# Kernel tuning notes

Hardware: AMD Instinct MI355X
Metric: run time of the kernel (lower is better)

The kernel has to match this reference:

```python
import jax, jax.numpy as jnp
import numpy as np

R = 0.9        # ball-query radius
K = 32         # max neighbors per ball
STRIDE = 4     # spatial stride -> M = N // STRIDE reference points
EPS = 1e-5     # BatchNorm eps


def fps(xyz, m):
    """Furthest point sampling (pointnet2 semantics: start at index 0).
    xyz: (N,3) -> (m,) int32 indices."""
    N = xyz.shape[0]

    def step(carry, _):
        dist, last = carry
        d = jnp.sum((xyz - xyz[last]) ** 2, axis=-1)
        dist = jnp.minimum(dist, d)
        nxt = jnp.argmax(dist).astype(jnp.int32)
        return (dist, nxt), nxt

    init = (jnp.full((N,), 1e10, dtype=xyz.dtype), jnp.int32(0))
    _, rest = jax.lax.scan(step, init, None, length=m - 1)
    return jnp.concatenate([jnp.zeros((1,), jnp.int32), rest])


def sample_group(xyz):
    """FPS + ball query + grouping for one frame. xyz: (N,3).
    Returns ref (M,3), disp4 (M,K,4)."""
    N = xyz.shape[0]
    m = N // STRIDE
    fi = fps(xyz, m)
    ref = xyz[fi]                                              # (M,3)
    d2 = jnp.sum((ref[:, None, :] - xyz[None, :, :]) ** 2, -1)  # (M,N)
    # pointnet2 ball_query: first K in-radius indices (original order),
    # positions without a neighbor padded with the first found index.
    cand = jnp.where(d2 < R * R, jnp.arange(N, dtype=jnp.int32)[None, :], N)
    idx = jnp.sort(cand, axis=1)[:, :K]                        # (M,K)
    idx = jnp.where(idx == N, idx[:, :1], idx)
    nb = xyz[idx]                                              # (M,K,3)
    disp = nb - ref[:, None, :]
    disp4 = jnp.concatenate([disp, jnp.zeros_like(disp[..., :1])], axis=-1)
    return ref, disp4


def batch_norm(h, gamma, beta):
    # torch BN (training-mode) per frame: stats over (B, M, K) per t.
    # h: (B,T,M,K,C)
    mean = jnp.mean(h, axis=(0, 2, 3), keepdims=True)
    var = jnp.mean((h - mean) ** 2, axis=(0, 2, 3), keepdims=True)
    return gamma * (h - mean) * jax.lax.rsqrt(var + EPS) + beta


def setup_inputs() -> dict:
    key = jax.random.key(0)
    ks = jax.random.split(key, 7)
    B, T, N = 2, 8, 4096
    C1, C2 = 64, 128
    return {
        "xyzs": jax.random.normal(ks[0], (B, T, N, 3), dtype=jnp.float32),
        "W1": jax.random.normal(ks[1], (C1, 4), dtype=jnp.float32) * 0.1,
        "g1": jnp.ones((C1,), jnp.float32),
        "b1": jnp.zeros((C1,), jnp.float32),
        "W2": jax.random.normal(ks[2], (C2, C1), dtype=jnp.float32) * 0.1,
        "g2": jnp.ones((C2,), jnp.float32),
        "b2": jnp.zeros((C2,), jnp.float32),
    }


def reference(xyzs, W1, g1, b1, W2, g2, b2):
    # xyzs: (B,T,N,3)
    ref, disp4 = jax.vmap(jax.vmap(sample_group))(xyzs)  # (B,T,M,3), (B,T,M,K,4)
    h = jnp.einsum('btmkc,oc->btmko', disp4, W1)         # conv_d 1x1
    h = jax.nn.relu(batch_norm(h, g1, b1))
    h = jnp.einsum('btmkc,oc->btmko', h, W2)             # mlp 1x1
    h = jax.nn.relu(batch_norm(h, g2, b2))
    feat = jnp.max(h, axis=3)                            # max over K -> (B,T,M,C)
    new_features = jnp.transpose(feat, (0, 1, 3, 2))     # (B,T,C,M) like torch
    return ref, new_features
```

## Files before the change

kernel.cpp:

```cpp
#include <hip/hip_runtime.h>
#include <hip/hip_bf16.h>


#define N_PTS   4096
#define M_PTS   1024
#define KNB     32

typedef _Float16 half8 __attribute__((ext_vector_type(8)));
typedef float    f32x4 __attribute__((ext_vector_type(4)));

__device__ inline float2 pk_sub(float2 a, float2 b) {
  float2 d;
  asm("v_pk_add_f32 %0, %1, %2 neg_lo:[0,1] neg_hi:[0,1]" : "=v"(d) : "v"(a), "v"(b));
  return d;
}
__device__ inline float2 pk_mul(float2 a, float2 b) {
  float2 d;
  asm("v_pk_mul_f32 %0, %1, %2" : "=v"(d) : "v"(a), "v"(b));
  return d;
}
__device__ inline float2 pk_add(float2 a, float2 b) {
  float2 d;
  asm("v_pk_add_f32 %0, %1, %2" : "=v"(d) : "v"(a), "v"(b));
  return d;
}

#define DPPMAXF(ctrl)                                                          \
  {                                                                            \
    unsigned _o = (unsigned)__builtin_amdgcn_update_dpp(                       \
        0, (int)__float_as_uint(m), (ctrl), 0xF, 0xF, true);                   \
    m = fmaxf(m, __uint_as_float(_o));                                         \
  }

__device__ inline float4 fold1_chan(const float* __restrict__ acc9, int t, int c,
                                    const float* __restrict__ W1,
                                    const float* __restrict__ g1,
                                    const float* __restrict__ b1) {
  const float inv_n = 1.0f / 65536.0f;
  const float* a = acc9 + t * 9;
  float mx = a[0] * inv_n, my = a[1] * inv_n, mz = a[2] * inv_n;
  float Sxx = a[3] * inv_n, Syy = a[4] * inv_n, Szz = a[5] * inv_n;
  float Sxy = a[6] * inv_n, Sxz = a[7] * inv_n, Syz = a[8] * inv_n;
  float w0 = W1[c * 4], w1 = W1[c * 4 + 1], w2 = W1[c * 4 + 2];
  float mean = w0 * mx + w1 * my + w2 * mz;
  float E2 = w0 * w0 * Sxx + w1 * w1 * Syy + w2 * w2 * Szz
           + 2.f * (w0 * w1 * Sxy + w0 * w2 * Sxz + w1 * w2 * Syz);
  float var = E2 - mean * mean;
  float al = g1[c] / sqrtf(var + 1e-5f);
  float4 o; o.x = w0 * al; o.y = w1 * al; o.z = w2 * al; o.w = b1[c] - mean * al;
  return o;
}

__global__ __launch_bounds__(512) void fps_kernel(const float* __restrict__ xyzs,
                                                  float* __restrict__ out) {
#pragma clang fp contract(off)
  const int bt  = blockIdx.x & 15;
  const int tid = threadIdx.x;
  __shared__ float sx[N_PTS], syy[N_PTS], szz[N_PTS];
  __shared__ unsigned long long sslot[2];
  __shared__ int sidx[M_PTS];

  const float* f = xyzs + (size_t)bt * (N_PTS * 3);
  for (int i = tid; i < N_PTS; i += 512) {
    sx[i]  = f[3 * i + 0];
    syy[i] = f[3 * i + 1];
    szz[i] = f[3 * i + 2];
  }
  if (tid == 0) { sidx[0] = 0; sslot[0] = 0ull; sslot[1] = 0ull; }
  __syncthreads();

  const int base = tid << 3;
  float2 px2[4], py2[4], pz2[4], dd2[4];
#pragma unroll
  for (int j = 0; j < 4; ++j) {
    int i0 = base + 2 * j;
    px2[j] = {sx[i0], sx[i0 + 1]};
    py2[j] = {syy[i0], syy[i0 + 1]};
    pz2[j] = {szz[i0], szz[i0 + 1]};
    dd2[j] = {1e10f, 1e10f};
  }
  float wx = sx[0], wy = syy[0], wz = szz[0];

  for (int it = 1; it < M_PTS; ++it) {
    float2 wxx = {wx, wx}, wyy = {wy, wy}, wzz = {wz, wz};
#pragma unroll
    for (int j = 0; j < 4; ++j) {
      float2 dx = pk_sub(px2[j], wxx);
      float2 dy = pk_sub(py2[j], wyy);
      float2 dz = pk_sub(pz2[j], wzz);
      float2 m1 = pk_mul(dx, dx);
      float2 m2 = pk_mul(dy, dy);
      float2 s  = pk_add(m1, m2);
      float2 m3 = pk_mul(dz, dz);
      float2 dt = pk_add(s, m3);
      dd2[j].x = fminf(dd2[j].x, dt.x);
      dd2[j].y = fminf(dd2[j].y, dt.y);
    }
    float v4[4]; int s4[4];
#pragma unroll
    for (int a = 0; a < 4; ++a) {
      bool t = dd2[a].y > dd2[a].x;
      v4[a] = t ? dd2[a].y : dd2[a].x;
      s4[a] = 2 * a + (t ? 1 : 0);
    }
    float v2[2]; int s2v[2];
#pragma unroll
    for (int a = 0; a < 2; ++a) {
      bool t = v4[2 * a + 1] > v4[2 * a];
      v2[a] = t ? v4[2 * a + 1] : v4[2 * a];
      s2v[a] = t ? s4[2 * a + 1] : s4[2 * a];
    }
    bool t1 = v2[1] > v2[0];
    float bv = t1 ? v2[1] : v2[0];
    int   bj = t1 ? s2v[1] : s2v[0];

    float m = bv;
    DPPMAXF(0x111);
    DPPMAXF(0x112);
    DPPMAXF(0x114);
    DPPMAXF(0x118);
    DPPMAXF(0x142);
    DPPMAXF(0x143);
    float vmax = __uint_as_float(
        (unsigned)__builtin_amdgcn_readlane((int)__float_as_uint(m), 63));

    const int p = it & 1;
    if (bv == vmax) {
      unsigned long long key = ((unsigned long long)(unsigned)it << 44)
          | ((unsigned long long)__float_as_uint(bv) << 12)
          | (unsigned long long)(4095u - (unsigned)((tid << 3) + bj));
      atomicMax(&sslot[p], key);
    }
    __syncthreads();
    unsigned long long kk = sslot[p];
    int bi = 4095 - (int)(kk & 0xFFFull);
    wx = sx[bi]; wy = syy[bi]; wz = szz[bi];
    if (tid == 0) sidx[it] = bi;
  }
  __syncthreads();
  float* orow = out + (size_t)bt * (M_PTS * 3);
  for (int i = tid; i < M_PTS; i += 512) {
    int ix = sidx[i];
    orow[3 * i + 0] = sx[ix];
    orow[3 * i + 1] = syy[ix];
    orow[3 * i + 2] = szz[ix];
  }
}

__global__ __launch_bounds__(256) void ball_stats(const float* __restrict__ xyzs,
                                                  const float* __restrict__ refpts,
                                                  float* __restrict__ disp4,
                                                  float* __restrict__ acc9) {
#pragma clang fp contract(off)
  const int tid  = threadIdx.x;
  const int lane = tid & 63, w = tid >> 6;
  const int gw   = (blockIdx.x << 2) + w;
  const int bt   = gw >> 10;
  const float* f = xyzs + (size_t)bt * (N_PTS * 3);
  const float* r = refpts + (size_t)gw * 3;
  const float rx = r[0], ry = r[1], rz = r[2];
  float* dout = disp4 + (size_t)gw * (KNB * 4);
  __shared__ float sred[4][9];

  float st[9];
#pragma unroll
  for (int q = 0; q < 9; ++q) st[q] = 0.f;

  int filled = 0;
  float p0x = 0.f, p0y = 0.f, p0z = 0.f;
  bool got0 = false;

  for (int base = 0; base < N_PTS; base += 64) {
    if (filled >= KNB) break;
    int j = base + lane;
    float x = f[3 * j], y = f[3 * j + 1], z = f[3 * j + 2];
    float dx = rx - x, dy = ry - y, dz = rz - z;
    float d2 = (dx * dx + dy * dy) + dz * dz;
    bool pred = d2 < 0.81f;
    unsigned long long mk = __ballot(pred);
    if (!got0 && mk) {
      int src = __builtin_ctzll(mk);
      p0x = __shfl(-dx, src); p0y = __shfl(-dy, src); p0z = __shfl(-dz, src);
      got0 = true;
    }
    int slot = filled + __popcll(mk & ((1ull << lane) - 1));
    if (pred && slot < KNB) {
      float vx = -dx, vy = -dy, vz = -dz;
      float4 v; v.x = vx; v.y = vy; v.z = vz; v.w = 0.f;
      *(float4*)(dout + slot * 4) = v;
      st[0] += vx;      st[1] += vy;      st[2] += vz;
      st[3] += vx * vx; st[4] += vy * vy; st[5] += vz * vz;
      st[6] += vx * vy; st[7] += vx * vz; st[8] += vy * vz;
    }
    filled += __popcll(mk);
  }
  if (filled < KNB) {
    for (int s = filled + lane; s < KNB; s += 64) {
      float4 v; v.x = p0x; v.y = p0y; v.z = p0z; v.w = 0.f;
      *(float4*)(dout + s * 4) = v;
    }
    if (lane == 0) {
      float cf = (float)(KNB - filled);
      st[0] += cf * p0x;       st[1] += cf * p0y;       st[2] += cf * p0z;
      st[3] += cf * p0x * p0x; st[4] += cf * p0y * p0y; st[5] += cf * p0z * p0z;
      st[6] += cf * p0x * p0y; st[7] += cf * p0x * p0z; st[8] += cf * p0y * p0z;
    }
  }
#pragma unroll
  for (int q = 0; q < 9; ++q) {
#pragma unroll
    for (int off = 1; off < 64; off <<= 1) st[q] += __shfl_xor(st[q], off);
  }
  if (lane == 0) {
#pragma unroll
    for (int q = 0; q < 9; ++q) sred[w][q] = st[q];
  }
  __syncthreads();
  if (tid < 9) {
    float v = sred[0][tid] + sred[1][tid] + sred[2][tid] + sred[3][tid];
    atomicAdd(&acc9[(bt & 7) * 9 + tid], v);
  }
}

__global__ __launch_bounds__(256) void gram_mfma(
    const float* __restrict__ disp4, const float* __restrict__ acc9,
    const float* __restrict__ W1, const float* __restrict__ g1,
    const float* __restrict__ b1,
    float* __restrict__ sumy, float* __restrict__ G) {
  const int t = blockIdx.x >> 5, chunk = blockIdx.x & 31;
  const int tid = threadIdx.x;
  const int lane = tid & 63, w = tid >> 6;
  __shared__ float4    sdisp[32];
  __shared__ _Float16  yt[2048];
  __shared__ float     red[256];

  const int c = lane;
  float4 wc = fold1_chan(acc9, t, c, W1, g1, b1);
  const int wswz = w ^ (c & 3) ^ ((c >> 2) & 3) ^ ((c >> 4) & 3);
  _Float16* wp = (_Float16*)((char*)yt + c * 64 + wswz * 16);

  f32x4 g0 = {0.f,0.f,0.f,0.f}, g1a = {0.f,0.f,0.f,0.f};
  f32x4 g2a = {0.f,0.f,0.f,0.f}, g3 = {0.f,0.f,0.f,0.f};
  float ysum = 0.f;

  const int frc = lane & 15, kg = lane >> 4;
  const int fsw = kg ^ (lane & 3) ^ ((lane >> 2) & 3);

  for (int b = 0; b < 64; ++b) {
    int sb = (chunk << 11) + (b << 5);
    if (tid < 32) {
      int smp = sb + tid;
      size_t flat = ((size_t)(smp >> 15) << 18) + ((size_t)t << 15) + (smp & 32767);
      sdisp[tid] = ((const float4*)disp4)[flat];
    }
    __syncthreads();
    half8 hv;
#pragma unroll
    for (int u = 0; u < 8; ++u) {
      float4 d = sdisp[w * 8 + u];
      float y = wc.x * d.x + wc.y * d.y + wc.z * d.z + wc.w;
      y = y > 0.f ? y : 0.f;
      ysum += y;
      hv[u] = (_Float16)y;
    }
    *(half8*)wp = hv;
    __syncthreads();
    half8 fA = *(const half8*)((const char*)yt + (16 * w + frc) * 64 + ((fsw ^ w) * 16));
    half8 f0 = *(const half8*)((const char*)yt + (frc) * 64       + ((fsw ^ 0) * 16));
    half8 f1 = *(const half8*)((const char*)yt + (16 + frc) * 64  + ((fsw ^ 1) * 16));
    half8 f2 = *(const half8*)((const char*)yt + (32 + frc) * 64  + ((fsw ^ 2) * 16));
    half8 f3 = *(const half8*)((const char*)yt + (48 + frc) * 64  + ((fsw ^ 3) * 16));
    g0  = __builtin_amdgcn_mfma_f32_16x16x32_f16(fA, f0, g0, 0, 0, 0);
    g1a = __builtin_amdgcn_mfma_f32_16x16x32_f16(fA, f1, g1a, 0, 0, 0);
    g2a = __builtin_amdgcn_mfma_f32_16x16x32_f16(fA, f2, g2a, 0, 0, 0);
    g3  = __builtin_amdgcn_mfma_f32_16x16x32_f16(fA, f3, g3, 0, 0, 0);
    __syncthreads();
  }
  red[tid] = ysum;
  __syncthreads();
  if (tid < 64) {
    float v = red[tid] + red[tid + 64] + red[tid + 128] + red[tid + 192];
    atomicAdd(&sumy[t * 64 + tid], v);
  }
  float* Gp = G + t * 4096;
  const int rbase = 16 * w + (lane >> 4) * 4, cb = lane & 15;
#pragma unroll
  for (int r2 = 0; r2 < 4; ++r2) {
    atomicAdd(&Gp[(rbase + r2) * 64 + cb],      g0[r2]);
    atomicAdd(&Gp[(rbase + r2) * 64 + 16 + cb], g1a[r2]);
    atomicAdd(&Gp[(rbase + r2) * 64 + 32 + cb], g2a[r2]);
    atomicAdd(&Gp[(rbase + r2) * 64 + 48 + cb], g3[r2]);
  }
}

__global__ __launch_bounds__(256) void fold2_kernel(const float* __restrict__ G,
    const float* __restrict__ sumy, const float* __restrict__ W2,
    const float* __restrict__ g2, const float* __restrict__ b2,
    _Float16* __restrict__ w2ph, float* __restrict__ beta2) {
  const int gidx = blockIdx.x * 256 + threadIdx.x;
  const int t = gidx >> 7, c2 = gidx & 127;
  const float inv_n = 1.f / 65536.f;
  const float* w = W2 + c2 * 64;
  float wreg[64];
#pragma unroll
  for (int q = 0; q < 16; ++q) {
    float4 v = ((const float4*)w)[q];
    wreg[4 * q] = v.x; wreg[4 * q + 1] = v.y; wreg[4 * q + 2] = v.z; wreg[4 * q + 3] = v.w;
  }
  float mean2 = 0.f;
#pragma unroll
  for (int j = 0; j < 64; ++j) mean2 += wreg[j] * (sumy[t * 64 + j] * inv_n);
  const float* Gp = G + t * 4096;
  float E2 = 0.f;
  for (int i = 0; i < 64; ++i) {
    const float* gr = Gp + i * 64;
    float gw = 0.f;
#pragma unroll
    for (int j = 0; j < 64; j += 4) {
      float4 gv = *(const float4*)&gr[j];
      gw += gv.x * wreg[j] + gv.y * wreg[j + 1] + gv.z * wreg[j + 2] + gv.w * wreg[j + 3];
    }
    E2 += wreg[i] * gw;
  }
  E2 *= inv_n;
  float var = E2 - mean2 * mean2;
  float al = g2[c2] / sqrtf(var + 1e-5f);
  float be = b2[c2] - mean2 * al;
  beta2[t * 128 + c2] = be;
  _Float16* wo = w2ph + (size_t)(t * 128 + c2) * 64;
#pragma unroll
  for (int j = 0; j < 64; ++j) wo[j] = (_Float16)(al * wreg[j]);
}

__global__ __launch_bounds__(256) void final_mfma(
    const float* __restrict__ disp4, const float* __restrict__ acc9,
    const float* __restrict__ W1, const float* __restrict__ g1,
    const float* __restrict__ b1,
    const _Float16* __restrict__ w2ph, const float* __restrict__ beta2,
    float* __restrict__ outfeat) {
  const int bid = blockIdx.x;
  const int bt = bid >> 6, mg = bid & 63;
  const int t = bt & 7;
  const int tid = threadIdx.x;
  const int lane = tid & 63, w = tid >> 6;

  __shared__ float4    sdisp[512];
  __shared__ _Float16  sy[512 * 64];

  {
    const float4* src = (const float4*)disp4 + (((size_t)(bt << 10) + (mg << 4)) << 5);
    sdisp[tid] = src[tid];
    sdisp[tid + 256] = src[tid + 256];
  }
  const int c0 = (tid & 31) * 2;
  float4 w1a = fold1_chan(acc9, t, c0, W1, g1, b1);
  float4 w1b = fold1_chan(acc9, t, c0 + 1, W1, g1, b1);
  __syncthreads();

  {
    const int r0 = (tid >> 5) * 64;
    const int hg = c0 >> 3;
    const int cin = (c0 & 7) * 2;
#pragma unroll 4
    for (int rr = 0; rr < 64; ++rr) {
      int row = r0 + rr;
      float4 d = sdisp[row];
      float ya = fmaxf(w1a.x * d.x + w1a.y * d.y + w1a.z * d.z + w1a.w, 0.f);
      float yb = fmaxf(w1b.x * d.x + w1b.y * d.y + w1b.z * d.z + w1b.w, 0.f);
      _Float16* p = (_Float16*)((char*)sy + row * 128 + ((hg ^ (row & 7)) * 16) + cin);
      p[0] = (_Float16)ya;
      p[1] = (_Float16)yb;
    }
  }
  __syncthreads();

  const int col = lane & 15, kg = lane >> 4;
  for (int ct = 0; ct < 8; ++ct) {
    const _Float16* wb = w2ph + ((size_t)(t * 128 + ct * 16 + col)) * 64 + kg * 8;
    half8 bf0 = *(const half8*)wb;
    half8 bf1 = *(const half8*)(wb + 32);
    float b2v = beta2[t * 128 + ct * 16 + col];
#pragma unroll
    for (int mi = 0; mi < 4; ++mi) {
      float mx = -1e30f;
#pragma unroll
      for (int h = 0; h < 2; ++h) {
        int row = (8 * w + 2 * mi + h) * 16 + col;
        int rm = row & 7;
        const char* rb = (const char*)sy + row * 128;
        half8 a0 = *(const half8*)(rb + ((kg ^ rm) * 16));
        half8 a1 = *(const half8*)(rb + (((4 + kg) ^ rm) * 16));
        f32x4 acc = {0.f, 0.f, 0.f, 0.f};
        acc = __builtin_amdgcn_mfma_f32_16x16x32_f16(a0, bf0, acc, 0, 0, 0);
        acc = __builtin_amdgcn_mfma_f32_16x16x32_f16(a1, bf1, acc, 0, 0, 0);
        float z = fmaxf(fmaxf(acc[0], acc[1]), fmaxf(acc[2], acc[3]));
        mx = fmaxf(mx, z);
      }
      mx = fmaxf(mx, __shfl_xor(mx, 16));
      mx = fmaxf(mx, __shfl_xor(mx, 32));
      if (lane < 16) {
        float v = fmaxf(mx + b2v, 0.f);
        int m = (mg << 4) + 4 * w + mi;
        outfeat[((size_t)(bt * 128 + ct * 16 + lane)) * 1024 + m] = v;
      }
    }
  }
}

extern "C" void kernel_launch(void* const* d_in, const int* in_sizes, int n_in,
                              void* d_out, int out_size, void* d_ws, size_t ws_size,
                              hipStream_t stream) {
  const float* xyzs = (const float*)d_in[0];
  const float* W1   = (const float*)d_in[1];
  const float* g1   = (const float*)d_in[2];
  const float* b1   = (const float*)d_in[3];
  const float* W2   = (const float*)d_in[4];
  const float* g2   = (const float*)d_in[5];
  const float* b2   = (const float*)d_in[6];
  float* out = (float*)d_out;
  float* ws  = (float*)d_ws;

  float*     disp4 = ws;
  float*     acc   = ws + 2097152;
  float*     sumy  = ws + 2097224;
  float*     G     = ws + 2097736;
  _Float16*  w2ph  = (_Float16*)(ws + 2130504);
  float*     beta2 = ws + 2163272;

  hipMemsetAsync(acc, 0, (72 + 512 + 32768) * sizeof(float), stream);
  fps_kernel  <<<256,  512, 0, stream>>>(xyzs, out);
  ball_stats  <<<4096, 256, 0, stream>>>(xyzs, out, disp4, acc);
  gram_mfma   <<<256,  256, 0, stream>>>(disp4, acc, W1, g1, b1, sumy, G);
  fold2_kernel<<<4,    256, 0, stream>>>(G, sumy, W2, g2, b2, w2ph, beta2);
  final_mfma  <<<1024, 256, 0, stream>>>(disp4, acc, W1, g1, b1, w2ph, beta2, out + 49152);
}
```

Measured before the change: 996.0 us.

## Broadcast FPS winner coords via LDS; enlarge gram_mfma tile to 256 samples

In FPS, the first lane of each wave that holds that wave's maximum writes its candidate coordinates to a small LDS array. After the barrier, every thread picks the winning wave's coordinates from that array instead of doing a dependent lookup into the point arrays with the winning index. In gram_mfma, each iteration now loads 256 samples instead of 32, with a larger LDS tile and a new swizzle. This runs 8 MFMA k-steps per barrier pair and cuts the loop from 64 to 8 rounds, reducing synchronisation overhead at the cost of more LDS use, which may lower occupancy.

Result: slower. 2.472 ms (+148.2%).

```diff
diff --git a/kernel.cpp b/kernel.cpp
--- a/kernel.cpp
+++ b/kernel.cpp
@@ -58,6 +58,7 @@
   const int tid = threadIdx.x;
   __shared__ float sx[N_PTS], syy[N_PTS], szz[N_PTS];
   __shared__ unsigned long long sslot[2];
+  __shared__ float4 scand[2][8];
   __shared__ int sidx[M_PTS];
 
   const float* f = xyzs + (size_t)bt * (N_PTS * 3);
@@ -124,18 +125,42 @@
     float vmax = __uint_as_float(
         (unsigned)__builtin_amdgcn_readlane((int)__float_as_uint(m), 63));
 
+    unsigned long long mk = __ballot(bv == vmax);
     const int p = it & 1;
-    if (bv == vmax) {
+    if ((tid & 63) == (int)__builtin_ctzll(mk)) {
+      float2 ax = (bj & 4) ? ((bj & 2) ? px2[3] : px2[2])
+                           : ((bj & 2) ? px2[1] : px2[0]);
+      float2 ay = (bj & 4) ? ((bj & 2) ? py2[3] : py2[2])
+                           : ((bj & 2) ? py2[1] : py2[0]);
+      float2 az = (bj & 4) ? ((bj & 2) ? pz2[3] : pz2[2])
+                           : ((bj & 2) ? pz2[1] : pz2[0]);
+      float4 cc;
+      cc.x = (bj & 1) ? ax.y : ax.x;
+      cc.y = (bj & 1) ? ay.y : ay.x;
+      cc.z = (bj & 1) ? az.y : az.x;
+      cc.w = 0.f;
+      scand[p][tid >> 6] = cc;
+      unsigned gi = (unsigned)((tid << 3) + bj);
       unsigned long long key = ((unsigned long long)(unsigned)it << 44)
           | ((unsigned long long)__float_as_uint(bv) << 12)
-          | (unsigned long long)(4095u - (unsigned)((tid << 3) + bj));
+          | (unsigned long long)(4095u - gi);
       atomicMax(&sslot[p], key);
     }
     __syncthreads();
+    float4 c0 = scand[p][0], c1 = scand[p][1], c2 = scand[p][2], c3 = scand[p][3];
+    float4 c4 = scand[p][4], c5 = scand[p][5], c6 = scand[p][6], c7 = scand[p][7];
     unsigned long long kk = sslot[p];
-    int bi = 4095 - (int)(kk & 0xFFFull);
-    wx = sx[bi]; wy = syy[bi]; wz = szz[bi];
-    if (tid == 0) sidx[it] = bi;
+    int gi_w = 4095 - (int)(kk & 0xFFFull);
+    int wv = gi_w >> 9;
+    float4 a0 = (wv & 1) ? c1 : c0;
+    float4 a1 = (wv & 1) ? c3 : c2;
+    float4 a2 = (wv & 1) ? c5 : c4;
+    float4 a3 = (wv & 1) ? c7 : c6;
+    float4 b0 = (wv & 2) ? a1 : a0;
+    float4 b1 = (wv & 2) ? a3 : a2;
+    float4 cw = (wv & 4) ? b1 : b0;
+    wx = cw.x; wy = cw.y; wz = cw.z;
+    if (tid == 0) sidx[it] = gi_w;
   }
   __syncthreads();
   float* orow = out + (size_t)bt * (M_PTS * 3);
@@ -230,50 +255,53 @@
   const int t = blockIdx.x >> 5, chunk = blockIdx.x & 31;
   const int tid = threadIdx.x;
   const int lane = tid & 63, w = tid >> 6;
-  __shared__ float4    sdisp[32];
-  __shared__ _Float16  yt[2048];
+  __shared__ float4    sdisp[256];
+  __shared__ _Float16  yt[64 * 256];
   __shared__ float     red[256];
 
   const int c = lane;
   float4 wc = fold1_chan(acc9, t, c, W1, g1, b1);
-  const int wswz = w ^ (c & 3) ^ ((c >> 2) & 3) ^ ((c >> 4) & 3);
-  _Float16* wp = (_Float16*)((char*)yt + c * 64 + wswz * 16);
-
   f32x4 g0 = {0.f,0.f,0.f,0.f}, g1a = {0.f,0.f,0.f,0.f};
   f32x4 g2a = {0.f,0.f,0.f,0.f}, g3 = {0.f,0.f,0.f,0.f};
   float ysum = 0.f;
-
   const int frc = lane & 15, kg = lane >> 4;
-  const int fsw = kg ^ (lane & 3) ^ ((lane >> 2) & 3);
-
-  for (int b = 0; b < 64; ++b) {
-    int sb = (chunk << 11) + (b << 5);
-    if (tid < 32) {
-      int smp = sb + tid;
-      size_t flat = ((size_t)(smp >> 15) << 18) + ((size_t)t << 15) + (smp & 32767);
-      sdisp[tid] = ((const float4*)disp4)[flat];
-    }
+  const int fsw = frc & 7;
+
+  for (int rnd = 0; rnd < 8; ++rnd) {
+    int smp = (chunk << 11) + (rnd << 8) + tid;
+    size_t flat = ((size_t)(smp >> 15) << 18) + ((size_t)t << 15) + (smp & 32767);
+    sdisp[tid] = ((const float4*)disp4)[flat];
     __syncthreads();
-    half8 hv;
-#pragma unroll
-    for (int u = 0; u < 8; ++u) {
-      float4 d = sdisp[w * 8 + u];
-      float y = wc.x * d.x + wc.y * d.y + wc.z * d.z + wc.w;
-      y = y > 0.f ? y : 0.f;
-      ysum += y;
-      hv[u] = (_Float16)y;
-    }
-    *(half8*)wp = hv;
+    char* rowb = (char*)yt + c * 512;
+    const int cs = c & 7;
+#pragma unroll
+    for (int u8 = 0; u8 < 8; ++u8) {
+      half8 hv;
+#pragma unroll
+      for (int u = 0; u < 8; ++u) {
+        float4 d = sdisp[(w << 6) + (u8 << 3) + u];
+        float y = wc.x * d.x + wc.y * d.y + wc.z * d.z + wc.w;
+        y = y > 0.f ? y : 0.f;
+        ysum += y;
+        hv[u] = (_Float16)y;
+      }
+      int g = (w << 3) + u8;
+      *(half8*)(rowb + (((g ^ cs)) << 4)) = hv;
+    }
     __syncthreads();
-    half8 fA = *(const half8*)((const char*)yt + (16 * w + frc) * 64 + ((fsw ^ w) * 16));
-    half8 f0 = *(const half8*)((const char*)yt + (frc) * 64       + ((fsw ^ 0) * 16));
-    half8 f1 = *(const half8*)((const char*)yt + (16 + frc) * 64  + ((fsw ^ 1) * 16));
-    half8 f2 = *(const half8*)((const char*)yt + (32 + frc) * 64  + ((fsw ^ 2) * 16));
-    half8 f3 = *(const half8*)((const char*)yt + (48 + frc) * 64  + ((fsw ^ 3) * 16));
-    g0  = __builtin_amdgcn_mfma_f32_16x16x32_f16(fA, f0, g0, 0, 0, 0);
-    g1a = __builtin_amdgcn_mfma_f32_16x16x32_f16(fA, f1, g1a, 0, 0, 0);
-    g2a = __builtin_amdgcn_mfma_f32_16x16x32_f16(fA, f2, g2a, 0, 0, 0);
-    g3  = __builtin_amdgcn_mfma_f32_16x16x32_f16(fA, f3, g3, 0, 0, 0);
+#pragma unroll
+    for (int ss = 0; ss < 8; ++ss) {
+      int gg = (ss << 2) + kg;
+      half8 fA = *(const half8*)((char*)yt + ((16 * w + frc) << 9) + ((gg ^ fsw) << 4));
+      half8 f0 = *(const half8*)((char*)yt + ((frc) << 9)          + ((gg ^ fsw) << 4));
+      half8 f1 = *(const half8*)((char*)yt + ((16 + frc) << 9)     + ((gg ^ fsw) << 4));
+      half8 f2 = *(const half8*)((char*)yt + ((32 + frc) << 9)     + ((gg ^ fsw) << 4));
+      half8 f3 = *(const half8*)((char*)yt + ((48 + frc) << 9)     + ((gg ^ fsw) << 4));
+      g0  = __builtin_amdgcn_mfma_f32_16x16x32_f16(fA, f0, g0, 0, 0, 0);
+      g1a = __builtin_amdgcn_mfma_f32_16x16x32_f16(fA, f1, g1a, 0, 0, 0);
+      g2a = __builtin_amdgcn_mfma_f32_16x16x32_f16(fA, f2, g2a, 0, 0, 0);
+      g3  = __builtin_amdgcn_mfma_f32_16x16x32_f16(fA, f3, g3, 0, 0, 0);
+    }
     __syncthreads();
   }
   red[tid] = ysum;
```
